# Kernel tuning notes

Hardware: AMD Instinct MI355X
Metric: run time of the kernel (lower is better)

The kernel has to match this reference:

```python
import jax, jax.numpy as jnp
import numpy as np

COMMITMENT_COST = 0.25
DECAY = 0.99
EPSILON = 1e-05


def setup_inputs() -> dict:
    key = jax.random.key(0)
    k1, k2, k3 = jax.random.split(key, 3)
    B, C, H, W = 64, 64, 64, 64  # C == embedding_dim
    K, D = 1024, 64
    return {
        "inputs": jax.random.normal(k1, (B, C, H, W), dtype=jnp.float32),
        "weight": jax.random.normal(k2, (K, D), dtype=jnp.float32),
        "ema_cluster_size": jnp.ones((K,), dtype=jnp.float32),
        "ema_w": jax.random.normal(k3, (K, D), dtype=jnp.float32),
    }


def reference(inputs, weight, ema_cluster_size, ema_w):
    K, D = weight.shape
    # NCHW -> NHWC, flatten to [N, D]
    x = jnp.transpose(inputs, (0, 2, 3, 1))
    flat = x.reshape(-1, D)
    # squared L2 distances to all codebook entries: [N, K]
    distances = (
        jnp.sum(flat * flat, axis=1, keepdims=True)
        + jnp.sum(weight * weight, axis=1)
        - 2.0 * flat @ weight.T
    )
    idx = jnp.argmin(distances, axis=1)  # [N]
    # training-mode EMA update (replaces the one-hot scatter + matmuls with segment sums)
    counts = jax.ops.segment_sum(jnp.ones_like(idx, dtype=flat.dtype), idx, num_segments=K)
    dw = jax.ops.segment_sum(flat, idx, num_segments=K)  # encodings.T @ flat_input
    cs = ema_cluster_size * DECAY + (1.0 - DECAY) * counts
    n = jnp.sum(cs)
    cs = (cs + EPSILON) / (n + K * EPSILON) * n  # Laplace smoothing
    ew = ema_w * DECAY + (1.0 - DECAY) * dw
    new_weight = ew / cs[:, None]
    # quantize with the UPDATED codebook (matches in-place torch order)
    quantized = new_weight[idx].reshape(x.shape)
    e_latent_loss = jnp.mean(jnp.square(jax.lax.stop_gradient(quantized) - x))
    loss = COMMITMENT_COST * e_latent_loss
    quantized_st = x + jax.lax.stop_gradient(quantized - x)  # straight-through
    return loss, jnp.transpose(quantized_st, (0, 3, 1, 2)), idx[:, None]
```

## Files before the change

### kernel.cpp

```cpp
#include <hip/hip_runtime.h>

#define K_CODES 1024
#define D_DIM   64
#define N_ROWS  262144
#define HW      4096
#define CHW     262144
#define N_ELEM  16777216
#define DECAY   0.99f
#define OMD     0.01f
#define EPS_F   1e-05f
#define MARGIN_BF 0.006f
#define FLAG_CAP 32768
#define SEG_CAP  2048
#define NHB      64

typedef __attribute__((ext_vector_type(8))) short bf16x8;
typedef __attribute__((ext_vector_type(4))) float f32x4;

constexpr size_t OFF_LOSS    = 0;
constexpr size_t OFF_FLAGCNT = 8;
constexpr size_t ZERO_BYTES  = 64;
constexpr size_t OFF_W2F     = 64;
constexpr size_t OFF_W2D     = 4160;
constexpr size_t OFF_CS     = 12352;
constexpr size_t OFF_GOFF    = 16448;
constexpr size_t OFF_DW      = 20608;
constexpr size_t OFF_NEWW    = 282752;
constexpr size_t OFF_IDX     = 544896;
constexpr size_t OFF_HISTB   = 1593472;
constexpr size_t OFF_SORT    = 1855616;
constexpr size_t OFF_FLAGS   = 1855616;
constexpr size_t OFF_WFRAG   = 1986688;

__device__ __forceinline__ short f2bf(float f) {
    unsigned u = __float_as_uint(f);
    u += 0x7fffu + ((u >> 16) & 1u);
    return (short)(u >> 16);
}
__device__ __forceinline__ float bf2f(short h) {
    return __uint_as_float(((unsigned)(unsigned short)h) << 16);
}

__device__ __forceinline__ void gload_lds16(const float4* g, void* l) {
    __builtin_amdgcn_global_load_lds(
        (const __attribute__((address_space(1))) void*)g,
        (__attribute__((address_space(3))) void*)l, 16, 0, 0);
}

__global__ __launch_bounds__(256) void prep_kernel(
    const float* __restrict__ w, short* __restrict__ wfrag,
    float* __restrict__ w2f, double* __restrict__ w2d) {
    int t = threadIdx.x;
    if (blockIdx.x < 32) {
        int gid = blockIdx.x * 256 + t;
        int j = gid >> 7, h = (gid >> 6) & 1, L = gid & 63;
        int code = j * 16 + (L & 15);
        int kb = h * 32 + ((L >> 4) << 3);
        const float* wp = w + code * D_DIM + kb;
        short hi[8], lo[8];
#pragma unroll
        for (int i = 0; i < 8; ++i) {
            float v = wp[i];
            short hb = f2bf(v);
            hi[i] = hb;
            lo[i] = f2bf(v - bf2f(hb));
        }
        short* dh = wfrag + (size_t)(((j * 2 + h) * 2 + 0) * 64 + L) * 8;
        short* dl = wfrag + (size_t)(((j * 2 + h) * 2 + 1) * 64 + L) * 8;
#pragma unroll
        for (int i = 0; i < 8; ++i) { dh[i] = hi[i]; dl[i] = lo[i]; }
    } else {
        int k = (blockIdx.x - 32) * 256 + t;
        const float* wk = w + k * D_DIM;
        float sf = 0.f; double sd = 0.0;
#pragma unroll
        for (int d = 0; d < D_DIM; ++d) {
            float wv = wk[d];
            sf = fmaf(wv, wv, sf);
            sd = fma((double)wv, (double)wv, sd);
        }
        w2f[k] = sf; w2d[k] = sd;
    }
}

__global__ __launch_bounds__(256) __attribute__((amdgpu_waves_per_eu(2, 4)))
void argmin_kernel(
    const float* __restrict__ inp, const short* __restrict__ wfrag,
    const float* __restrict__ w2f, int* __restrict__ idx_ws,
    float* __restrict__ out_idx_f, float* __restrict__ xt,
    int* __restrict__ flagcnt, int* __restrict__ flaglist) {
    __shared__ float w2s[K_CODES];
    __shared__ alignas(16) char smem_u[64 * 68 * 4];
    __shared__ alignas(16) short bufA[8192];
    float (*xs)[68] = (float (*)[68])smem_u;
    short* bufB = (short*)smem_u;

    int t = threadIdx.x;
    ((float4*)w2s)[t] = ((const float4*)w2f)[t];

    int rowbase = blockIdx.x * 64;
    int b = rowbase >> 12, hwb = rowbase & (HW - 1);
    const float* xp = inp + (size_t)b * CHW + hwb;
    int lane = t & 63, wave = t >> 6;
#pragma unroll
    for (int it = 0; it < 16; ++it) {
        int d = wave * 16 + it;
        xs[lane][d] = xp[(size_t)d * HW + lane];
    }
    __syncthreads();

    float4* xt4 = (float4*)(xt + (size_t)rowbase * D_DIM);
#pragma unroll
    for (int i2 = 0; i2 < 4; ++i2) {
        int c2 = t + i2 * 256;
        xt4[c2] = ((const float4*)xs[c2 >> 4])[c2 & 15];
    }

    int q = lane >> 4, col = lane & 15;
    int rl = wave * 16 + col;
    bf16x8 ah0, ah1, al0, al1;
#pragma unroll
    for (int i = 0; i < 8; ++i) {
        float v0 = xs[rl][q * 8 + i];
        short h0 = f2bf(v0);
        ah0[i] = h0; al0[i] = f2bf(v0 - bf2f(h0));
        float v1 = xs[rl][q * 8 + 32 + i];
        short h1 = f2bf(v1);
        ah1[i] = h1; al1[i] = f2bf(v1 - bf2f(h1));
    }

    float best[4]  = {3.4e38f, 3.4e38f, 3.4e38f, 3.4e38f};
    float best2[4] = {3.4e38f, 3.4e38f, 3.4e38f, 3.4e38f};
    int   bk[4]    = {0, 0, 0, 0};
    const float4* wsrc = (const float4*)wfrag;

    {
        const float4* src = wsrc + t;
        char* nb = (char*)bufA + wave * 1024;
#pragma unroll
        for (int i2 = 0; i2 < 4; ++i2)
            gload_lds16(src + i2 * 256, nb + i2 * 4096);
    }

    for (int st = 0; st < 16; ++st) {
        asm volatile("s_waitcnt vmcnt(0)" ::: "memory");
        __syncthreads();
        if (st < 15) {
            const float4* src = wsrc + (size_t)(st + 1) * 1024 + t;
            char* nb = ((st & 1) ? (char*)bufA : (char*)bufB) + wave * 1024;
#pragma unroll
            for (int i2 = 0; i2 < 4; ++i2)
                gload_lds16(src + i2 * 256, nb + i2 * 4096);
        }
        const bf16x8* wt = (const bf16x8*)((st & 1) ? bufB : bufA);

#pragma unroll
        for (int jj = 0; jj < 4; ++jj) {
            int j = st * 4 + jj;
            bf16x8 bh0 = wt[(jj * 4 + 0) * 64 + lane];
            bf16x8 bl0 = wt[(jj * 4 + 1) * 64 + lane];
            bf16x8 bh1 = wt[(jj * 4 + 2) * 64 + lane];
            bf16x8 bl1 = wt[(jj * 4 + 3) * 64 + lane];
            f32x4 acc = {0.f, 0.f, 0.f, 0.f};
            acc = __builtin_amdgcn_mfma_f32_16x16x32_bf16(al0, bh0, acc, 0, 0, 0);
            acc = __builtin_amdgcn_mfma_f32_16x16x32_bf16(al1, bh1, acc, 0, 0, 0);
            acc = __builtin_amdgcn_mfma_f32_16x16x32_bf16(ah0, bl0, acc, 0, 0, 0);
            acc = __builtin_amdgcn_mfma_f32_16x16x32_bf16(ah1, bl1, acc, 0, 0, 0);
            acc = __builtin_amdgcn_mfma_f32_16x16x32_bf16(ah0, bh0, acc, 0, 0, 0);
            acc = __builtin_amdgcn_mfma_f32_16x16x32_bf16(ah1, bh1, acc, 0, 0, 0);
            float w2c = w2s[j * 16 + col];
            int c = j * 16 + col;
#pragma unroll
            for (int r = 0; r < 4; ++r) {
                float s = fmaf(-2.f, acc[r], w2c);
                bool lt = s < best[r];
                best2[r] = fminf(best2[r], fmaxf(s, best[r]));
                best[r]  = fminf(best[r], s);
                bk[r]    = lt ? c : bk[r];
            }
        }
    }

#pragma unroll
    for (int m = 1; m < 16; m <<= 1) {
#pragma unroll
        for (int r = 0; r < 4; ++r) {
            float ob  = __shfl_xor(best[r], m, 64);
            float ob2 = __shfl_xor(best2[r], m, 64);
            int   obk = __shfl_xor(bk[r], m, 64);
            float nb2 = fminf(fminf(best2[r], ob2), fmaxf(best[r], ob));
            int   nbk = ob < best[r] ? obk
                        : (best[r] < ob ? bk[r] : min(bk[r], obk));
            best[r]  = fminf(best[r], ob);
            best2[r] = nb2;
            bk[r]    = nbk;
        }
    }

    if (col == 0) {
#pragma unroll
        for (int r = 0; r < 4; ++r) {
            int row = rowbase + wave * 16 + q * 4 + r;
            idx_ws[row]    = bk[r];
            out_idx_f[row] = (float)bk[r];
            if (best2[r] - best[r] < MARGIN_BF) {
                int pos = atomicAdd(flagcnt, 1);
                if (pos < FLAG_CAP) flaglist[pos] = row;
            }
        }
    }
}

__global__ __launch_bounds__(256) void refine_kernel(
    const float* __restrict__ xt, const float* __restrict__ weight,
    const double* __restrict__ w2d, int* __restrict__ idx_ws,
    float* __restrict__ out_idx_f, const int* __restrict__ flagcnt,
    const int* __restrict__ flaglist) {
    int cnt = *flagcnt;
    if (cnt > FLAG_CAP) cnt = FLAG_CAP;

    __shared__ float  sx[D_DIM];
    __shared__ double sd[256];
    __shared__ int    si[256];
    int t = threadIdx.x;

    for (int r = blockIdx.x; r < cnt; r += gridDim.x) {
        int row = flaglist[r];
        if (t < D_DIM) sx[t] = xt[(size_t)row * D_DIM + t];
        __syncthreads();

        double x2 = 0.0;
#pragma unroll
        for (int d = 0; d < D_DIM; ++d) {
            double xv = (double)sx[d];
            x2 = fma(xv, xv, x2);
        }

        double bd = 1.0e300; int bi = 0;
#pragma unroll
        for (int jj = 0; jj < 4; ++jj) {
            int k = t + jj * 256;
            const float* wk = weight + k * D_DIM;
            double dot = 0.0;
#pragma unroll
            for (int d = 0; d < D_DIM; ++d)
                dot = fma((double)wk[d], (double)sx[d], dot);
            double dist = (x2 + w2d[k]) - 2.0 * dot;
            if (dist < bd) { bd = dist; bi = k; }
        }
        sd[t] = bd; si[t] = bi;
        __syncthreads();
        for (int s = 128; s > 0; s >>= 1) {
            if (t < s) {
                double od = sd[t + s]; int oi = si[t + s];
                if (od < sd[t] || (od == sd[t] && oi < si[t])) {
                    sd[t] = od; si[t] = oi;
                }
            }
            __syncthreads();
        }
        if (t == 0 && si[0] != idx_ws[row]) {
            idx_ws[row]    = si[0];
            out_idx_f[row] = (float)si[0];
        }
        __syncthreads();
    }
}

__global__ __launch_bounds__(256) void hist_kernel(
    const int* __restrict__ idx_ws, int* __restrict__ histb) {
    __shared__ int h[K_CODES];
    int t = threadIdx.x, b = blockIdx.x;
    for (int i = t; i < K_CODES; i += 256) h[i] = 0;
    __syncthreads();
    const int4* idx4 = (const int4*)idx_ws + b * 1024;
#pragma unroll
    for (int i = 0; i < 4; ++i) {
        int4 c = idx4[t + i * 256];
        atomicAdd(&h[c.x], 1); atomicAdd(&h[c.y], 1);
        atomicAdd(&h[c.z], 1); atomicAdd(&h[c.w], 1);
    }
    __syncthreads();
    for (int i = t; i < K_CODES; i += 256) histb[b * K_CODES + i] = h[i];
}

__global__ __launch_bounds__(1024) void scan_kernel(
    int* __restrict__ histb, int* __restrict__ goff,
    const float* __restrict__ ema_cs, float* __restrict__ csbuf) {
    __shared__ int pre[K_CODES];
    __shared__ float red[K_CODES];
    int k = threadIdx.x;

    int s = 0;
    for (int b = 0; b < NHB; ++b) {
        int v = histb[b * K_CODES + k];
        histb[b * K_CODES + k] = s;
        s += v;
    }
    int cnt = s;

    pre[k] = cnt;
    __syncthreads();
    for (int d = 1; d < K_CODES; d <<= 1) {
        int v = (k >= d) ? pre[k - d] : 0;
        __syncthreads();
        if (k >= d) pre[k] += v;
        __syncthreads();
    }
    int base = pre[k] - cnt;
    goff[k] = base;
    if (k == K_CODES - 1) goff[K_CODES] = pre[k];

    for (int b = 0; b < NHB; ++b) histb[b * K_CODES + k] += base;

    float cs = ema_cs[k] * DECAY + OMD * (float)cnt;
    red[k] = cs;
    __syncthreads();
    for (int s2 = 512; s2 > 0; s2 >>= 1) {
        if (k < s2) red[k] += red[k + s2];
        __syncthreads();
    }
    float n = red[0];
    csbuf[k] = (cs + EPS_F) / (n + (float)K_CODES * EPS_F) * n;
}

__global__ __launch_bounds__(256) void scatter_kernel(
    const int* __restrict__ idx_ws, const int* __restrict__ histb,
    int* __restrict__ sorted) {
    __shared__ int cur[K_CODES];
    int t = threadIdx.x, b = blockIdx.x;
    for (int i = t; i < K_CODES; i += 256) cur[i] = histb[b * K_CODES + i];
    __syncthreads();
    const int4* idx4 = (const int4*)idx_ws + b * 1024;
#pragma unroll
    for (int i = 0; i < 4; ++i) {
        int4 c = idx4[t + i * 256];
        int r0 = (b * 1024 + t + i * 256) * 4;
        sorted[atomicAdd(&cur[c.x], 1)] = r0 + 0;
        sorted[atomicAdd(&cur[c.y], 1)] = r0 + 1;
        sorted[atomicAdd(&cur[c.z], 1)] = r0 + 2;
        sorted[atomicAdd(&cur[c.w], 1)] = r0 + 3;
    }
}

__global__ __launch_bounds__(256) void dwred_kernel(
    const float* __restrict__ xt, const int* __restrict__ sorted,
    const int* __restrict__ goff, float* __restrict__ dw) {
    __shared__ int   rows[SEG_CAP];
    __shared__ float red[256];
    int k = blockIdx.x, t = threadIdx.x;
    int base = goff[k];
    int cnt = goff[k + 1] - base;
    int cc = cnt > SEG_CAP ? SEG_CAP : cnt;

    for (int i = t; i < cc; i += 256) rows[i] = sorted[base + i];
    __syncthreads();

    int d = t & 63, sub = t >> 6;
    float a0 = 0.f, a1 = 0.f;
    int i = sub;
    for (; i + 4 < cc; i += 8) {
        a0 += xt[(size_t)rows[i] * D_DIM + d];
        a1 += xt[(size_t)rows[i + 4] * D_DIM + d];
    }
    for (; i < cc; i += 4) a0 += xt[(size_t)rows[i] * D_DIM + d];
    red[t] = a0 + a1;
    __syncthreads();
    if (t < 64) {
        dw[k * D_DIM + t] = red[t] + red[t + 64] + red[t + 128] + red[t + 192];
    }
}

__global__ __launch_bounds__(256) void emaw_kernel(
    const float* __restrict__ ema_w, const float* __restrict__ dw,
    const float* __restrict__ csbuf, float* __restrict__ new_w) {
    int i = blockIdx.x * 256 + threadIdx.x;
    new_w[i] = (ema_w[i] * DECAY + OMD * dw[i]) / csbuf[i >> 6];
}

__global__ __launch_bounds__(256) void out_kernel(
    const float* __restrict__ inp, const float* __restrict__ new_w,
    const int* __restrict__ idx_ws, float* __restrict__ out,
    double* __restrict__ loss_acc) {
    int row = blockIdx.x * 256 + threadIdx.x;
    int b  = row >> 12;
    int hw = row & (HW - 1);
    const float* xp = inp + (size_t)b * CHW + hw;
    float* op = out + 1 + (size_t)b * CHW + hw;

    int k = idx_ws[row];
    const float* q = new_w + k * D_DIM;

    float lsum = 0.f;
#pragma unroll
    for (int d = 0; d < D_DIM; ++d) {
        float xv = xp[(size_t)d * HW];
        float qv = q[d];
        float diff = qv - xv;
        lsum = fmaf(diff, diff, lsum);
        op[(size_t)d * HW] = xv + diff;
    }

    __shared__ double lred[256];
    lred[threadIdx.x] = (double)lsum;
    __syncthreads();
    for (int s = 128; s > 0; s >>= 1) {
        if (threadIdx.x < s) lred[threadIdx.x] += lred[threadIdx.x + s];
        __syncthreads();
    }
    if (threadIdx.x == 0) atomicAdd(loss_acc, lred[0]);
}

__global__ void loss_final(const double* __restrict__ loss_acc,
                           float* __restrict__ out) {
    out[0] = (float)(0.25 * (*loss_acc / (double)N_ELEM));
}

extern "C" void kernel_launch(void* const* d_in, const int* in_sizes, int n_in,
                              void* d_out, int out_size, void* d_ws, size_t ws_size,
                              hipStream_t stream) {
    const float* inp    = (const float*)d_in[0];
    const float* weight = (const float*)d_in[1];
    const float* ema_cs = (const float*)d_in[2];
    const float* ema_w  = (const float*)d_in[3];
    float* out = (float*)d_out;

    char* ws = (char*)d_ws;
    double* loss_acc = (double*)(ws + OFF_LOSS);
    int*    flagcnt  = (int*)(ws + OFF_FLAGCNT);
    float*  w2f      = (float*)(ws + OFF_W2F);
    double* w2d      = (double*)(ws + OFF_W2D);
    float*  csbuf    = (float*)(ws + OFF_CS);
    int*    goff     = (int*)(ws + OFF_GOFF);
    float*  dw       = (float*)(ws + OFF_DW);
    float*  new_w    = (float*)(ws + OFF_NEWW);
    int*    idx_ws   = (int*)(ws + OFF_IDX);
    int*    histb    = (int*)(ws + OFF_HISTB);
    int*    sorted   = (int*)(ws + OFF_SORT);
    int*    flaglist = (int*)(ws + OFF_FLAGS);
    short*  wfrag    = (short*)(ws + OFF_WFRAG);

    float* xt        = out + 1;
    float* out_idx_f = out + 1 + (size_t)N_ELEM;

    hipMemsetAsync(ws, 0, ZERO_BYTES, stream);

    prep_kernel<<<36, 256, 0, stream>>>(weight, wfrag, w2f, w2d);

    argmin_kernel<<<N_ROWS / 64, 256, 0, stream>>>(
        inp, wfrag, w2f, idx_ws, out_idx_f, xt, flagcnt, flaglist);

    refine_kernel<<<1024, 256, 0, stream>>>(
        xt, weight, w2d, idx_ws, out_idx_f, flagcnt, flaglist);

    hist_kernel<<<NHB, 256, 0, stream>>>(idx_ws, histb);

    scan_kernel<<<1, 1024, 0, stream>>>(histb, goff, ema_cs, csbuf);

    scatter_kernel<<<NHB, 256, 0, stream>>>(idx_ws, histb, sorted);

    dwred_kernel<<<K_CODES, 256, 0, stream>>>(xt, sorted, goff, dw);

    emaw_kernel<<<K_CODES * D_DIM / 256, 256, 0, stream>>>(ema_w, dw, csbuf, new_w);

    out_kernel<<<N_ROWS / 256, 256, 0, stream>>>(inp, new_w, idx_ws, out, loss_acc);

    loss_final<<<1, 1, 0, stream>>>(loss_acc, out);
}
```

Before: 446.1 us.

## Process 128 rows per argmin block, pack index into key, fuse EMA and loss kernels

```diff
diff --git a/kernel.cpp b/kernel.cpp
--- a/kernel.cpp
+++ b/kernel.cpp
@@ -9,16 +9,18 @@
 #define DECAY   0.99f
 #define OMD     0.01f
 #define EPS_F   1e-05f
-#define MARGIN_BF 0.006f
+#define MARGIN_BF 0.008f
 #define FLAG_CAP 32768
 #define SEG_CAP  2048
 #define NHB      64
+#define BROWS    128
 
 typedef __attribute__((ext_vector_type(8))) short bf16x8;
 typedef __attribute__((ext_vector_type(4))) float f32x4;
 
 constexpr size_t OFF_LOSS    = 0;
 constexpr size_t OFF_FLAGCNT = 8;
+constexpr size_t OFF_DONE    = 12;
 constexpr size_t ZERO_BYTES  = 64;
 constexpr size_t OFF_W2F     = 64;
 constexpr size_t OFF_W2D     = 4160;
@@ -90,7 +92,7 @@
     float* __restrict__ out_idx_f, float* __restrict__ xt,
     int* __restrict__ flagcnt, int* __restrict__ flaglist) {
     __shared__ float w2s[K_CODES];
-    __shared__ alignas(16) char smem_u[64 * 68 * 4];
+    __shared__ alignas(16) char smem_u[BROWS * 68 * 4];
     __shared__ alignas(16) short bufA[8192];
     float (*xs)[68] = (float (*)[68])smem_u;
     short* bufB = (short*)smem_u;
@@ -98,40 +100,49 @@
     int t = threadIdx.x;
     ((float4*)w2s)[t] = ((const float4*)w2f)[t];
 
-    int rowbase = blockIdx.x * 64;
+    int rowbase = blockIdx.x * BROWS;
     int b = rowbase >> 12, hwb = rowbase & (HW - 1);
     const float* xp = inp + (size_t)b * CHW + hwb;
     int lane = t & 63, wave = t >> 6;
-#pragma unroll
-    for (int it = 0; it < 16; ++it) {
-        int d = wave * 16 + it;
-        xs[lane][d] = xp[(size_t)d * HW + lane];
+
+    int sr = t & 127, sd = t >> 7;
+#pragma unroll
+    for (int it = 0; it < 32; ++it) {
+        int d = it * 2 + sd;
+        xs[sr][d] = xp[(size_t)d * HW + sr];
     }
     __syncthreads();
 
     float4* xt4 = (float4*)(xt + (size_t)rowbase * D_DIM);
 #pragma unroll
-    for (int i2 = 0; i2 < 4; ++i2) {
+    for (int i2 = 0; i2 < 8; ++i2) {
         int c2 = t + i2 * 256;
         xt4[c2] = ((const float4*)xs[c2 >> 4])[c2 & 15];
     }
 
     int q = lane >> 4, col = lane & 15;
-    int rl = wave * 16 + col;
-    bf16x8 ah0, ah1, al0, al1;
-#pragma unroll
-    for (int i = 0; i < 8; ++i) {
-        float v0 = xs[rl][q * 8 + i];
-        short h0 = f2bf(v0);
-        ah0[i] = h0; al0[i] = f2bf(v0 - bf2f(h0));
-        float v1 = xs[rl][q * 8 + 32 + i];
-        short h1 = f2bf(v1);
-        ah1[i] = h1; al1[i] = f2bf(v1 - bf2f(h1));
-    }
-
-    float best[4]  = {3.4e38f, 3.4e38f, 3.4e38f, 3.4e38f};
-    float best2[4] = {3.4e38f, 3.4e38f, 3.4e38f, 3.4e38f};
-    int   bk[4]    = {0, 0, 0, 0};
+    int wavebase = wave * 32;
+    bf16x8 aH[2][2], aL[2][2];
+#pragma unroll
+    for (int s2 = 0; s2 < 2; ++s2) {
+        int rl = wavebase + s2 * 16 + col;
+#pragma unroll
+        for (int h = 0; h < 2; ++h) {
+#pragma unroll
+            for (int i = 0; i < 8; ++i) {
+                float v = xs[rl][h * 32 + q * 8 + i];
+                short hb = f2bf(v);
+                aH[s2][h][i] = hb;
+                aL[s2][h][i] = f2bf(v - bf2f(hb));
+            }
+        }
+    }
+
+    float best[2][4], best2[2][4];
+#pragma unroll
+    for (int s2 = 0; s2 < 2; ++s2)
+#pragma unroll
+        for (int r = 0; r < 4; ++r) { best[s2][r] = 3.4e38f; best2[s2][r] = 3.4e38f; }
     const float4* wsrc = (const float4*)wfrag;
 
     {
@@ -161,51 +172,75 @@
             bf16x8 bl0 = wt[(jj * 4 + 1) * 64 + lane];
             bf16x8 bh1 = wt[(jj * 4 + 2) * 64 + lane];
             bf16x8 bl1 = wt[(jj * 4 + 3) * 64 + lane];
-            f32x4 acc = {0.f, 0.f, 0.f, 0.f};
-            acc = __builtin_amdgcn_mfma_f32_16x16x32_bf16(al0, bh0, acc, 0, 0, 0);
-            acc = __builtin_amdgcn_mfma_f32_16x16x32_bf16(al1, bh1, acc, 0, 0, 0);
-            acc = __builtin_amdgcn_mfma_f32_16x16x32_bf16(ah0, bl0, acc, 0, 0, 0);
-            acc = __builtin_amdgcn_mfma_f32_16x16x32_bf16(ah1, bl1, acc, 0, 0, 0);
-            acc = __builtin_amdgcn_mfma_f32_16x16x32_bf16(ah0, bh0, acc, 0, 0, 0);
-            acc = __builtin_amdgcn_mfma_f32_16x16x32_bf16(ah1, bh1, acc, 0, 0, 0);
+            f32x4 acc0 = {0.f, 0.f, 0.f, 0.f};
+            f32x4 acc1 = {0.f, 0.f, 0.f, 0.f};
+            acc0 = __builtin_amdgcn_mfma_f32_16x16x32_bf16(aL[0][0], bh0, acc0, 0, 0, 0);
+            acc1 = __builtin_amdgcn_mfma_f32_16x16x32_bf16(aL[1][0], bh0, acc1, 0, 0, 0);
+            acc0 = __builtin_amdgcn_mfma_f32_16x16x32_bf16(aL[0][1], bh1, acc0, 0, 0, 0);
+            acc1 = __builtin_amdgcn_mfma_f32_16x16x32_bf16(aL[1][1], bh1, acc1, 0, 0, 0);
+            acc0 = __builtin_amdgcn_mfma_f32_16x16x32_bf16(aH[0][0], bl0, acc0, 0, 0, 0);
+            acc1 = __builtin_amdgcn_mfma_f32_16x16x32_bf16(aH[1][0], bl0, acc1, 0, 0, 0);
+            acc0 = __builtin_amdgcn_mfma_f32_16x16x32_bf16(aH[0][1], bl1, acc0, 0, 0, 0);
+            acc1 = __builtin_amdgcn_mfma_f32_16x16x32_bf16(aH[1][1], bl1, acc1, 0, 0, 0);
+            acc0 = __builtin_amdgcn_mfma_f32_16x16x32_bf16(aH[0][0], bh0, acc0, 0, 0, 0);
+            acc1 = __builtin_amdgcn_mfma_f32_16x16x32_bf16(aH[1][0], bh0, acc1, 0, 0, 0);
+            acc0 = __builtin_amdgcn_mfma_f32_16x16x32_bf16(aH[0][1], bh1, acc0, 0, 0, 0);
+            acc1 = __builtin_amdgcn_mfma_f32_16x16x32_bf16(aH[1][1], bh1, acc1, 0, 0, 0);
             float w2c = w2s[j * 16 + col];
-            int c = j * 16 + col;
+#pragma unroll
+            for (int s2 = 0; s2 < 2; ++s2) {
+#pragma unroll
+                for (int r = 0; r < 4; ++r) {
+                    float s = fmaf(-2.f, (s2 ? acc1 : acc0)[r], w2c);
+                    float key = __int_as_float(
+                        (__float_as_int(s) & ~63) | j);
+                    best2[s2][r] = fminf(best2[s2][r], fmaxf(key, best[s2][r]));
+                    best[s2][r]  = fminf(best[s2][r], key);
+                }
+            }
+        }
+    }
+
+    int bk[2][4];
+#pragma unroll
+    for (int s2 = 0; s2 < 2; ++s2)
+#pragma unroll
+        for (int r = 0; r < 4; ++r)
+            bk[s2][r] = ((__float_as_int(best[s2][r]) & 63) << 4) | col;
+
+#pragma unroll
+    for (int m = 1; m < 16; m <<= 1) {
+#pragma unroll
+        for (int s2 = 0; s2 < 2; ++s2) {
 #pragma unroll
             for (int r = 0; r < 4; ++r) {
-                float s = fmaf(-2.f, acc[r], w2c);
-                bool lt = s < best[r];
-                best2[r] = fminf(best2[r], fmaxf(s, best[r]));
-                best[r]  = fminf(best[r], s);
-                bk[r]    = lt ? c : bk[r];
+                float ob  = __shfl_xor(best[s2][r], m, 64);
+                float ob2 = __shfl_xor(best2[s2][r], m, 64);
+                int   obk = __shfl_xor(bk[s2][r], m, 64);
+                float nb2 = fminf(fminf(best2[s2][r], ob2),
+                                  fmaxf(best[s2][r], ob));
+                int   nbk = ob < best[s2][r] ? obk
+                            : (best[s2][r] < ob ? bk[s2][r]
+                                                : min(bk[s2][r], obk));
+                best[s2][r]  = fminf(best[s2][r], ob);
+                best2[s2][r] = nb2;
+                bk[s2][r]    = nbk;
             }
         }
     }
 
-#pragma unroll
-    for (int m = 1; m < 16; m <<= 1) {
-#pragma unroll
-        for (int r = 0; r < 4; ++r) {
-            float ob  = __shfl_xor(best[r], m, 64);
-            float ob2 = __shfl_xor(best2[r], m, 64);
-            int   obk = __shfl_xor(bk[r], m, 64);
-            float nb2 = fminf(fminf(best2[r], ob2), fmaxf(best[r], ob));
-            int   nbk = ob < best[r] ? obk
-                        : (best[r] < ob ? bk[r] : min(bk[r], obk));
-            best[r]  = fminf(best[r], ob);
-            best2[r] = nb2;
-            bk[r]    = nbk;
-        }
-    }
-
     if (col == 0) {
 #pragma unroll
-        for (int r = 0; r < 4; ++r) {
-            int row = rowbase + wave * 16 + q * 4 + r;
-            idx_ws[row]    = bk[r];
-            out_idx_f[row] = (float)bk[r];
-            if (best2[r] - best[r] < MARGIN_BF) {
-                int pos = atomicAdd(flagcnt, 1);
-                if (pos < FLAG_CAP) flaglist[pos] = row;
+        for (int s2 = 0; s2 < 2; ++s2) {
+#pragma unroll
+            for (int r = 0; r < 4; ++r) {
+                int row = rowbase + wave * 32 + s2 * 16 + q * 4 + r;
+                idx_ws[row]    = bk[s2][r];
+                out_idx_f[row] = (float)bk[s2][r];
+                if (best2[s2][r] - best[s2][r] < MARGIN_BF) {
+                    int pos = atomicAdd(flagcnt, 1);
+                    if (pos < FLAG_CAP) flaglist[pos] = row;
+                }
             }
         }
     }
@@ -345,7 +380,8 @@
 
 __global__ __launch_bounds__(256) void dwred_kernel(
     const float* __restrict__ xt, const int* __restrict__ sorted,
-    const int* __restrict__ goff, float* __restrict__ dw) {
+    const int* __restrict__ goff, const float* __restrict__ ema_w,
+    const float* __restrict__ csbuf, float* __restrict__ new_w) {
     __shared__ int   rows[SEG_CAP];
     __shared__ float red[256];
     int k = blockIdx.x, t = threadIdx.x;
@@ -367,21 +403,16 @@
     red[t] = a0 + a1;
     __syncthreads();
     if (t < 64) {
-        dw[k * D_DIM + t] = red[t] + red[t + 64] + red[t + 128] + red[t + 192];
-    }
-}
-
-__global__ __launch_bounds__(256) void emaw_kernel(
-    const float* __restrict__ ema_w, const float* __restrict__ dw,
-    const float* __restrict__ csbuf, float* __restrict__ new_w) {
-    int i = blockIdx.x * 256 + threadIdx.x;
-    new_w[i] = (ema_w[i] * DECAY + OMD * dw[i]) / csbuf[i >> 6];
+        float dwv = red[t] + red[t + 64] + red[t + 128] + red[t + 192];
+        new_w[k * D_DIM + t] =
+            (ema_w[k * D_DIM + t] * DECAY + OMD * dwv) / csbuf[k];
+    }
 }
 
 __global__ __launch_bounds__(256) void out_kernel(
     const float* __restrict__ inp, const float* __restrict__ new_w,
     const int* __restrict__ idx_ws, float* __restrict__ out,
-    double* __restrict__ loss_acc) {
+    double* __restrict__ loss_acc, int* __restrict__ done_cnt) {
     int row = blockIdx.x * 256 + threadIdx.x;
     int b  = row >> 12;
     int hw = row & (HW - 1);
@@ -408,12 +439,15 @@
         if (threadIdx.x < s) lred[threadIdx.x] += lred[threadIdx.x + s];
         __syncthreads();
     }
-    if (threadIdx.x == 0) atomicAdd(loss_acc, lred[0]);
-}
-
-__global__ void loss_final(const double* __restrict__ loss_acc,
-                           float* __restrict__ out) {
-    out[0] = (float)(0.25 * (*loss_acc / (double)N_ELEM));
+    if (threadIdx.x == 0) {
+        atomicAdd(loss_acc, lred[0]);
+        __threadfence();
+        int old = atomicAdd(done_cnt, 1);
+        if (old == (int)gridDim.x - 1) {
+            double v = atomicAdd(loss_acc, 0.0);
+            out[0] = (float)(0.25 * (v / (double)N_ELEM));
+        }
+    }
 }
 
 extern "C" void kernel_launch(void* const* d_in, const int* in_sizes, int n_in,
@@ -428,11 +462,11 @@
     char* ws = (char*)d_ws;
     double* loss_acc = (double*)(ws + OFF_LOSS);
     int*    flagcnt  = (int*)(ws + OFF_FLAGCNT);
+    int*    done_cnt = (int*)(ws + OFF_DONE);
     float*  w2f      = (float*)(ws + OFF_W2F);
     double* w2d      = (double*)(ws + OFF_W2D);
     float*  csbuf    = (float*)(ws + OFF_CS);
     int*    goff     = (int*)(ws + OFF_GOFF);
-    float*  dw       = (float*)(ws + OFF_DW);
     float*  new_w    = (float*)(ws + OFF_NEWW);
     int*    idx_ws   = (int*)(ws + OFF_IDX);
     int*    histb    = (int*)(ws + OFF_HISTB);
@@ -447,7 +481,7 @@
 
     prep_kernel<<<36, 256, 0, stream>>>(weight, wfrag, w2f, w2d);
 
-    argmin_kernel<<<N_ROWS / 64, 256, 0, stream>>>(
+    argmin_kernel<<<N_ROWS / BROWS, 256, 0, stream>>>(
         inp, wfrag, w2f, idx_ws, out_idx_f, xt, flagcnt, flaglist);
 
     refine_kernel<<<1024, 256, 0, stream>>>(
@@ -459,11 +493,8 @@
 
     scatter_kernel<<<NHB, 256, 0, stream>>>(idx_ws, histb, sorted);
 
-    dwred_kernel<<<K_CODES, 256, 0, stream>>>(xt, sorted, goff, dw);
-
-    emaw_kernel<<<K_CODES * D_DIM / 256, 256, 0, stream>>>(ema_w, dw, csbuf, new_w);
-
-    out_kernel<<<N_ROWS / 256, 256, 0, stream>>>(inp, new_w, idx_ws, out, loss_acc);
-
-    loss_final<<<1, 1, 0, stream>>>(loss_acc, out);
-}
+    dwred_kernel<<<K_CODES, 256, 0, stream>>>(xt, sorted, goff, ema_w, csbuf, new_w);
+
+    out_kernel<<<N_ROWS / 256, 256, 0, stream>>>(inp, new_w, idx_ws, out,
+                                                 loss_acc, done_cnt);
+}
```

Measured after the change: 488.2 us. 1.09x slower.
